# Kernel tuning notes

Measured on AMD Instinct MI355X. Metric: run time of the kernel, lower is better.

The kernel has to match this reference:

```python
import jax, jax.numpy as jnp
import numpy as np

BETA = 0.9
THRESH = 1.0
SLOPE = 25.0  # snntorch surrogate.fast_sigmoid default slope
T_SNN = 20
ACTION_BOUND = 1.0


@jax.custom_vjp
def spike(x):
    # Heaviside forward, fast-sigmoid surrogate backward
    return (x > 0.0).astype(x.dtype)

def _spike_fwd(x):
    return spike(x), x

def _spike_bwd(x, g):
    return (g / (SLOPE * jnp.abs(x) + 1.0) ** 2,)

spike.defvjp(_spike_fwd, _spike_bwd)


def lif_step(mem, z):
    # snntorch Leaky, reset_mechanism='subtract': reset from PRE-update mem, detached
    reset = jax.lax.stop_gradient(spike(mem - THRESH)) * THRESH
    mem = BETA * mem + z - reset
    spk = spike(mem - THRESH)
    return spk, mem


def setup_inputs() -> dict:
    key = jax.random.key(0)
    ks = jax.random.split(key, 5)
    B, F, A = 8192, 256, 8
    std = 0.08
    return {
        "state": jax.random.normal(ks[0], (B, F), jnp.float32),
        "W1": jax.random.normal(ks[1], (256, F), jnp.float32) * std,
        "b1": jnp.full((256,), 0.05, jnp.float32),
        "W2": jax.random.normal(ks[2], (64, 256), jnp.float32) * std,
        "b2": jnp.full((64,), 0.05, jnp.float32),
        "Wmu": jax.random.normal(ks[3], (A, 64), jnp.float32) * std,
        "bmu": jnp.full((A,), 0.05, jnp.float32),
        "Wsig": jax.random.normal(ks[4], (A, 64), jnp.float32) * std,
        "bsig": jnp.full((A,), 0.05, jnp.float32),
    }


def reference(state, W1, b1, W2, b2, Wmu, bmu, Wsig, bsig):
    B = state.shape[0]
    A = Wmu.shape[0]
    dt = state.dtype
    # fc1(state) is identical every step in the original loop; hoist it.
    z1 = state @ W1.T + b1  # [B, 256]

    def step(carry, _):
        mem1, mem2, mem_mu, mem_sig = carry
        spk1, mem1 = lif_step(mem1, z1)
        z2 = spk1 @ W2.T + b2                    # [B, 64]
        spk2, mem2 = lif_step(mem2, z2)
        _, mem_mu = lif_step(mem_mu, spk2 @ Wmu.T + bmu)
        _, mem_sig = lif_step(mem_sig, spk2 @ Wsig.T + bsig)
        return (mem1, mem2, mem_mu, mem_sig), None

    init = (jnp.zeros((B, 256), dt), jnp.zeros((B, 64), dt),
            jnp.zeros((B, A), dt), jnp.zeros((B, A), dt))
    (mem1, mem2, mem_mu, mem_sig), _ = jax.lax.scan(step, init, None, length=T_SNN)

    mu = jnp.tanh(mem_mu) * ACTION_BOUND
    sigma = jax.nn.softplus(mem_sig) + 0.03
    mu = jnp.nan_to_num(mu, nan=0.0, posinf=ACTION_BOUND, neginf=-ACTION_BOUND)
    sigma = jnp.nan_to_num(sigma, nan=0.1, posinf=1.0, neginf=0.1)
    sigma = jnp.clip(sigma, 0.03, 1.0)
    return mu, sigma
```

## Files before the change

### kernel.cpp

```cpp
#include <hip/hip_runtime.h>
#include <cstdint>

#define T_SNN 20
#define THREADS 1024
#define ROWS 32
#define W2LD 268
#define WMLD 68

#define SGN64(M, BIT) ({ int64_t _s;                                         \
    asm("s_bfe_i64 %0, %1, %2" : "=s"(_s) : "s"(M), "n"((BIT) | 0x10000));   \
    (uint32_t)_s; })

__global__ __launch_bounds__(THREADS)
void snn_v8(const float* __restrict__ state,
            const float* __restrict__ W1,
            const float* __restrict__ b1,
            const float* __restrict__ W2,
            const float* __restrict__ b2,
            const float* __restrict__ Wmu,
            const float* __restrict__ bmu,
            const float* __restrict__ Wsig,
            const float* __restrict__ bsig,
            float* __restrict__ out, int B)
{
    __shared__ float z1s  [ROWS * 256];
    __shared__ float w2lds[64 * W2LD];
    __shared__ float wms2 [16 * WMLD];
    __shared__ float bms_s[16];

    const int tid  = threadIdx.x;
    const int row0 = blockIdx.x * ROWS;

    for (int e = tid; e < 64 * 256; e += THREADS) {
        int j = e >> 8, i = e & 255;
        w2lds[j * W2LD + i] = W2[e];
    }
    for (int e = tid; e < 16 * 64; e += THREADS) {
        int q = e >> 6, j = e & 63;
        wms2[q * WMLD + j] = (q < 8) ? Wmu[q * 64 + j] : Wsig[(q - 8) * 64 + j];
    }
    if (tid < 16) bms_s[tid] = (tid < 8) ? bmu[tid] : bsig[tid - 8];

    {
        const int i1 = tid & 255;
        const int h  = __builtin_amdgcn_readfirstlane((int)(threadIdx.x >> 8));
        const float* __restrict__ w1row = W1 + i1 * 256;
        const float* __restrict__ sg = state + (size_t)(row0 + h * 8) * 256;
        float acc[8];
        #pragma unroll
        for (int r = 0; r < 8; ++r) acc[r] = 0.f;
        for (int k = 0; k < 256; k += 4) {
            const float4 wv = *reinterpret_cast<const float4*>(w1row + k);
            #pragma unroll
            for (int r = 0; r < 8; ++r) {
                const float4 sv = *reinterpret_cast<const float4*>(sg + r * 256 + k);
                acc[r] = __fmaf_rn(sv.x, wv.x, acc[r]);
                acc[r] = __fmaf_rn(sv.y, wv.y, acc[r]);
                acc[r] = __fmaf_rn(sv.z, wv.z, acc[r]);
                acc[r] = __fmaf_rn(sv.w, wv.w, acc[r]);
            }
        }
        const float bb = b1[i1];
        #pragma unroll
        for (int r = 0; r < 8; ++r)
            z1s[(h * 8 + r) * 256 + i1] = __fadd_rn(acc[r], bb);
    }
    __syncthreads();

    if (tid >= 512) return;

    const int lane = tid & 63;
    const int wv_  = __builtin_amdgcn_readfirstlane((int)(threadIdx.x >> 6));
    const int rhat = lane >> 4;
    const int q    = lane & 15;

    float z1r[4][4], mem1[4][4];
    #pragma unroll
    for (int r = 0; r < 4; ++r)
        #pragma unroll
        for (int c = 0; c < 4; ++c) {
            z1r[r][c]  = z1s[(wv_ * 4 + r) * 256 + c * 64 + lane];
            mem1[r][c] = 0.f;
        }
    float mem2[4] = {0.f, 0.f, 0.f, 0.f};
    float m34 = 0.f;
    const float b2j  = b2[lane];
    const float bmsq = bms_s[q];

    #pragma unroll 1
    for (int t = 0; t < T_SNN; ++t) {
        uint64_t mk[4][4];
        #pragma unroll
        for (int r = 0; r < 4; ++r)
            #pragma unroll
            for (int c = 0; c < 4; ++c) {
                float rst = (mem1[r][c] > 1.0f) ? 1.0f : 0.0f;
                float a = __fmul_rn(0.9f, mem1[r][c]);
                a = __fadd_rn(a, z1r[r][c]);
                mem1[r][c] = __fsub_rn(a, rst);
                mk[r][c] = __ballot(mem1[r][c] > 1.0f);
            }

        float acc[4] = {0.f, 0.f, 0.f, 0.f};
        #pragma unroll
        for (int c = 0; c < 4; ++c) {
            #pragma unroll
            for (int wb = 0; wb < 8; ++wb) {
                const float4 wa = *reinterpret_cast<const float4*>(
                    &w2lds[lane * W2LD + c * 64 + wb * 8]);
                const float4 wb4 = *reinterpret_cast<const float4*>(
                    &w2lds[lane * W2LD + c * 64 + wb * 8 + 4]);
                #pragma unroll
                for (int r = 0; r < 4; ++r) {
                    const uint64_t m = mk[r][c];
                    acc[r] = __fadd_rn(acc[r], __uint_as_float(__float_as_uint(wa.x)  & SGN64(m, wb*8+0)));
                    acc[r] = __fadd_rn(acc[r], __uint_as_float(__float_as_uint(wa.y)  & SGN64(m, wb*8+1)));
                    acc[r] = __fadd_rn(acc[r], __uint_as_float(__float_as_uint(wa.z)  & SGN64(m, wb*8+2)));
                    acc[r] = __fadd_rn(acc[r], __uint_as_float(__float_as_uint(wa.w)  & SGN64(m, wb*8+3)));
                    acc[r] = __fadd_rn(acc[r], __uint_as_float(__float_as_uint(wb4.x) & SGN64(m, wb*8+4)));
                    acc[r] = __fadd_rn(acc[r], __uint_as_float(__float_as_uint(wb4.y) & SGN64(m, wb*8+5)));
                    acc[r] = __fadd_rn(acc[r], __uint_as_float(__float_as_uint(wb4.z) & SGN64(m, wb*8+6)));
                    acc[r] = __fadd_rn(acc[r], __uint_as_float(__float_as_uint(wb4.w) & SGN64(m, wb*8+7)));
                }
            }
        }

        uint64_t m2[4];
        #pragma unroll
        for (int r = 0; r < 4; ++r) {
            float z2  = __fadd_rn(acc[r], b2j);
            float rst = (mem2[r] > 1.0f) ? 1.0f : 0.0f;
            float a   = __fmul_rn(0.9f, mem2[r]);
            a = __fadd_rn(a, z2);
            mem2[r] = __fsub_rn(a, rst);
            m2[r] = __ballot(mem2[r] > 1.0f);
        }

        uint64_t msel = m2[0];
        if (rhat == 1) msel = m2[1];
        if (rhat == 2) msel = m2[2];
        if (rhat == 3) msel = m2[3];
        const uint32_t mlo = (uint32_t)msel, mhi = (uint32_t)(msel >> 32);

        float accm = 0.f;
        #pragma unroll
        for (int jw = 0; jw < 16; ++jw) {
            const float4 wvv = *reinterpret_cast<const float4*>(&wms2[q * WMLD + jw * 4]);
            #pragma unroll
            for (int e = 0; e < 4; ++e) {
                const int j = jw * 4 + e;
                const uint32_t mw = (j < 32) ? mlo : mhi;
                const int b = j & 31;
                const uint32_t sg = (uint32_t)(((int32_t)(mw << (31 - b))) >> 31);
                const float we = (e == 0) ? wvv.x : (e == 1) ? wvv.y : (e == 2) ? wvv.z : wvv.w;
                accm = __fadd_rn(accm, __uint_as_float(__float_as_uint(we) & sg));
            }
        }
        float zm  = __fadd_rn(accm, bmsq);
        float rst = (m34 > 1.0f) ? 1.0f : 0.0f;
        float a   = __fmul_rn(0.9f, m34);
        a = __fadd_rn(a, zm);
        m34 = __fsub_rn(a, rst);
    }

    const int row = row0 + wv_ * 4 + rhat;
    if (q < 8) {
        out[row * 8 + q] = (float)tanh((double)m34);
    } else {
        double mv = (double)m34;
        double sp = fmax(mv, 0.0) + log1p(exp(-fabs(mv)));
        double sg = fmin(fmax(sp + 0.03, 0.03), 1.0);
        out[(size_t)B * 8 + row * 8 + (q - 8)] = (float)sg;
    }
}

extern "C" void kernel_launch(void* const* d_in, const int* in_sizes, int n_in,
                              void* d_out, int out_size, void* d_ws, size_t ws_size,
                              hipStream_t stream) {
    const float* state = (const float*)d_in[0];
    const float* W1    = (const float*)d_in[1];
    const float* b1    = (const float*)d_in[2];
    const float* W2    = (const float*)d_in[3];
    const float* b2    = (const float*)d_in[4];
    const float* Wmu   = (const float*)d_in[5];
    const float* bmu   = (const float*)d_in[6];
    const float* Wsig  = (const float*)d_in[7];
    const float* bsig  = (const float*)d_in[8];
    float* out = (float*)d_out;

    const int B = in_sizes[0] / 256;
    hipLaunchKernelGGL(snn_v8, dim3(B / ROWS), dim3(THREADS), 0, stream,
                       state, W1, b1, W2, b2, Wmu, bmu, Wsig, bsig, out, B);
}
```

Measured before the change: 230.8 us.

## Run recurrent phase on all 16 waves with two rows per wave

```diff
diff --git a/kernel.cpp b/kernel.cpp
--- a/kernel.cpp
+++ b/kernel.cpp
@@ -12,7 +12,7 @@
     (uint32_t)_s; })
 
 __global__ __launch_bounds__(THREADS)
-void snn_v8(const float* __restrict__ state,
+void snn_v9(const float* __restrict__ state,
             const float* __restrict__ W1,
             const float* __restrict__ b1,
             const float* __restrict__ W2,
@@ -67,31 +67,30 @@
     }
     __syncthreads();
 
-    if (tid >= 512) return;
-
     const int lane = tid & 63;
     const int wv_  = __builtin_amdgcn_readfirstlane((int)(threadIdx.x >> 6));
-    const int rhat = lane >> 4;
+    const int rhat = (lane >> 4) & 1;
     const int q    = lane & 15;
 
-    float z1r[4][4], mem1[4][4];
+    float z1r[2][4], mem1[2][4];
     #pragma unroll
-    for (int r = 0; r < 4; ++r)
+    for (int r = 0; r < 2; ++r)
         #pragma unroll
         for (int c = 0; c < 4; ++c) {
-            z1r[r][c]  = z1s[(wv_ * 4 + r) * 256 + c * 64 + lane];
+            z1r[r][c]  = z1s[(wv_ * 2 + r) * 256 + c * 64 + lane];
             mem1[r][c] = 0.f;
         }
-    float mem2[4] = {0.f, 0.f, 0.f, 0.f};
+    float mem2[2] = {0.f, 0.f};
     float m34 = 0.f;
     const float b2j  = b2[lane];
     const float bmsq = bms_s[q];
+    const float* __restrict__ wp = &w2lds[lane * W2LD];
 
     #pragma unroll 1
     for (int t = 0; t < T_SNN; ++t) {
-        uint64_t mk[4][4];
-        #pragma unroll
-        for (int r = 0; r < 4; ++r)
+        uint64_t mk[2][4];
+        #pragma unroll
+        for (int r = 0; r < 2; ++r)
             #pragma unroll
             for (int c = 0; c < 4; ++c) {
                 float rst = (mem1[r][c] > 1.0f) ? 1.0f : 0.0f;
@@ -101,47 +100,53 @@
                 mk[r][c] = __ballot(mem1[r][c] > 1.0f);
             }
 
-        float acc[4] = {0.f, 0.f, 0.f, 0.f};
+        float acc0 = 0.f, acc1 = 0.f;
         #pragma unroll
         for (int c = 0; c < 4; ++c) {
+            const uint64_t m0 = mk[0][c], m1 = mk[1][c];
             #pragma unroll
             for (int wb = 0; wb < 8; ++wb) {
-                const float4 wa = *reinterpret_cast<const float4*>(
-                    &w2lds[lane * W2LD + c * 64 + wb * 8]);
-                const float4 wb4 = *reinterpret_cast<const float4*>(
-                    &w2lds[lane * W2LD + c * 64 + wb * 8 + 4]);
-                #pragma unroll
-                for (int r = 0; r < 4; ++r) {
-                    const uint64_t m = mk[r][c];
-                    acc[r] = __fadd_rn(acc[r], __uint_as_float(__float_as_uint(wa.x)  & SGN64(m, wb*8+0)));
-                    acc[r] = __fadd_rn(acc[r], __uint_as_float(__float_as_uint(wa.y)  & SGN64(m, wb*8+1)));
-                    acc[r] = __fadd_rn(acc[r], __uint_as_float(__float_as_uint(wa.z)  & SGN64(m, wb*8+2)));
-                    acc[r] = __fadd_rn(acc[r], __uint_as_float(__float_as_uint(wa.w)  & SGN64(m, wb*8+3)));
-                    acc[r] = __fadd_rn(acc[r], __uint_as_float(__float_as_uint(wb4.x) & SGN64(m, wb*8+4)));
-                    acc[r] = __fadd_rn(acc[r], __uint_as_float(__float_as_uint(wb4.y) & SGN64(m, wb*8+5)));
-                    acc[r] = __fadd_rn(acc[r], __uint_as_float(__float_as_uint(wb4.z) & SGN64(m, wb*8+6)));
-                    acc[r] = __fadd_rn(acc[r], __uint_as_float(__float_as_uint(wb4.w) & SGN64(m, wb*8+7)));
-                }
-            }
-        }
-
-        uint64_t m2[4];
-        #pragma unroll
-        for (int r = 0; r < 4; ++r) {
-            float z2  = __fadd_rn(acc[r], b2j);
-            float rst = (mem2[r] > 1.0f) ? 1.0f : 0.0f;
-            float a   = __fmul_rn(0.9f, mem2[r]);
+                const float4 wa  = *reinterpret_cast<const float4*>(wp + c * 64 + wb * 8);
+                const float4 wb4 = *reinterpret_cast<const float4*>(wp + c * 64 + wb * 8 + 4);
+                acc0 = __fadd_rn(acc0, __uint_as_float(__float_as_uint(wa.x)  & SGN64(m0, wb*8+0)));
+                acc1 = __fadd_rn(acc1, __uint_as_float(__float_as_uint(wa.x)  & SGN64(m1, wb*8+0)));
+                acc0 = __fadd_rn(acc0, __uint_as_float(__float_as_uint(wa.y)  & SGN64(m0, wb*8+1)));
+                acc1 = __fadd_rn(acc1, __uint_as_float(__float_as_uint(wa.y)  & SGN64(m1, wb*8+1)));
+                acc0 = __fadd_rn(acc0, __uint_as_float(__float_as_uint(wa.z)  & SGN64(m0, wb*8+2)));
+                acc1 = __fadd_rn(acc1, __uint_as_float(__float_as_uint(wa.z)  & SGN64(m1, wb*8+2)));
+                acc0 = __fadd_rn(acc0, __uint_as_float(__float_as_uint(wa.w)  & SGN64(m0, wb*8+3)));
+                acc1 = __fadd_rn(acc1, __uint_as_float(__float_as_uint(wa.w)  & SGN64(m1, wb*8+3)));
+                acc0 = __fadd_rn(acc0, __uint_as_float(__float_as_uint(wb4.x) & SGN64(m0, wb*8+4)));
+                acc1 = __fadd_rn(acc1, __uint_as_float(__float_as_uint(wb4.x) & SGN64(m1, wb*8+4)));
+                acc0 = __fadd_rn(acc0, __uint_as_float(__float_as_uint(wb4.y) & SGN64(m0, wb*8+5)));
+                acc1 = __fadd_rn(acc1, __uint_as_float(__float_as_uint(wb4.y) & SGN64(m1, wb*8+5)));
+                acc0 = __fadd_rn(acc0, __uint_as_float(__float_as_uint(wb4.z) & SGN64(m0, wb*8+6)));
+                acc1 = __fadd_rn(acc1, __uint_as_float(__float_as_uint(wb4.z) & SGN64(m1, wb*8+6)));
+                acc0 = __fadd_rn(acc0, __uint_as_float(__float_as_uint(wb4.w) & SGN64(m0, wb*8+7)));
+                acc1 = __fadd_rn(acc1, __uint_as_float(__float_as_uint(wb4.w) & SGN64(m1, wb*8+7)));
+            }
+        }
+
+        uint64_t m2[2];
+        {
+            float z2  = __fadd_rn(acc0, b2j);
+            float rst = (mem2[0] > 1.0f) ? 1.0f : 0.0f;
+            float a   = __fmul_rn(0.9f, mem2[0]);
             a = __fadd_rn(a, z2);
-            mem2[r] = __fsub_rn(a, rst);
-            m2[r] = __ballot(mem2[r] > 1.0f);
-        }
-
-        uint64_t msel = m2[0];
-        if (rhat == 1) msel = m2[1];
-        if (rhat == 2) msel = m2[2];
-        if (rhat == 3) msel = m2[3];
-        const uint32_t mlo = (uint32_t)msel, mhi = (uint32_t)(msel >> 32);
-
+            mem2[0] = __fsub_rn(a, rst);
+            m2[0] = __ballot(mem2[0] > 1.0f);
+        }
+        {
+            float z2  = __fadd_rn(acc1, b2j);
+            float rst = (mem2[1] > 1.0f) ? 1.0f : 0.0f;
+            float a   = __fmul_rn(0.9f, mem2[1]);
+            a = __fadd_rn(a, z2);
+            mem2[1] = __fsub_rn(a, rst);
+            m2[1] = __ballot(mem2[1] > 1.0f);
+        }
+
+        const uint32_t mlo = rhat ? (uint32_t)m2[1] : (uint32_t)m2[0];
+        const uint32_t mhi = rhat ? (uint32_t)(m2[1] >> 32) : (uint32_t)(m2[0] >> 32);
         float accm = 0.f;
         #pragma unroll
         for (int jw = 0; jw < 16; ++jw) {
@@ -150,8 +155,7 @@
             for (int e = 0; e < 4; ++e) {
                 const int j = jw * 4 + e;
                 const uint32_t mw = (j < 32) ? mlo : mhi;
-                const int b = j & 31;
-                const uint32_t sg = (uint32_t)(((int32_t)(mw << (31 - b))) >> 31);
+                const uint32_t sg = (uint32_t)__builtin_amdgcn_sbfe(mw, j & 31, 1);
                 const float we = (e == 0) ? wvv.x : (e == 1) ? wvv.y : (e == 2) ? wvv.z : wvv.w;
                 accm = __fadd_rn(accm, __uint_as_float(__float_as_uint(we) & sg));
             }
@@ -163,14 +167,16 @@
         m34 = __fsub_rn(a, rst);
     }
 
-    const int row = row0 + wv_ * 4 + rhat;
-    if (q < 8) {
-        out[row * 8 + q] = (float)tanh((double)m34);
-    } else {
-        double mv = (double)m34;
-        double sp = fmax(mv, 0.0) + log1p(exp(-fabs(mv)));
-        double sg = fmin(fmax(sp + 0.03, 0.03), 1.0);
-        out[(size_t)B * 8 + row * 8 + (q - 8)] = (float)sg;
+    if (lane < 32) {
+        const int row = row0 + wv_ * 2 + rhat;
+        if (q < 8) {
+            out[row * 8 + q] = (float)tanh((double)m34);
+        } else {
+            double mv = (double)m34;
+            double sp = fmax(mv, 0.0) + log1p(exp(-fabs(mv)));
+            double sg = fmin(fmax(sp + 0.03, 0.03), 1.0);
+            out[(size_t)B * 8 + row * 8 + (q - 8)] = (float)sg;
+        }
     }
 }
 
@@ -189,6 +195,6 @@
     float* out = (float*)d_out;
 
     const int B = in_sizes[0] / 256;
-    hipLaunchKernelGGL(snn_v8, dim3(B / ROWS), dim3(THREADS), 0, stream,
+    hipLaunchKernelGGL(snn_v9, dim3(B / ROWS), dim3(THREADS), 0, stream,
                        state, W1, b1, W2, b2, Wmu, bmu, Wsig, bsig, out, B);
 }
```

Result: faster. 189.2 us (-18.0%).
